# Optimization experiments

Measured on AMD Instinct MI355X. Metric: run time of the kernel, lower is better.

## Reference

```python
import jax, jax.numpy as jnp
import numpy as np

B, T, IN, H, OUT = 1024, 1024, 1, 20, 2
G = 4 * H  # gate dim (i, f, g, o order as in PyTorch)


def setup_inputs() -> dict:
    key = jax.random.key(0)
    ks = jax.random.split(key, 16)
    s = 1.0 / np.sqrt(H)  # PyTorch default uniform(-1/sqrt(H), 1/sqrt(H)) scale
    def u(k, shape):
        return jax.random.uniform(k, shape, jnp.float32, -s, s)
    inp = {"x": jax.random.normal(ks[0], (B, T, IN), jnp.float32)}
    ins = [IN, H, H]
    i = 1
    for l in range(3):
        inp[f"w_ih{l}"] = u(ks[i], (G, ins[l])); i += 1
        inp[f"w_hh{l}"] = u(ks[i], (G, H)); i += 1
        inp[f"b_ih{l}"] = u(ks[i], (G,)); i += 1
        inp[f"b_hh{l}"] = u(ks[i], (G,)); i += 1
    inp["fc_w"] = u(ks[13], (OUT, H))
    inp["fc_b"] = u(ks[14], (OUT,))
    return inp


def _lstm_layer(x, w_ih, w_hh, b_ih, b_hh):
    # x: [B, T, in] -> hidden sequence [B, T, H]
    b, t, _ = x.shape
    h = w_hh.shape[1]
    # Precompute input contribution for all timesteps (vectorized over T).
    xg = jnp.einsum('bti,gi->btg', x, w_ih) + b_ih + b_hh  # [B, T, 4H]

    def step(carry, xg_t):
        hp, cp = carry
        gates = xg_t + hp @ w_hh.T  # [B, 4H]
        i, f, g, o = jnp.split(gates, 4, axis=-1)
        c = jax.nn.sigmoid(f) * cp + jax.nn.sigmoid(i) * jnp.tanh(g)
        hn = jax.nn.sigmoid(o) * jnp.tanh(c)
        return (hn, c), hn

    h0 = jnp.zeros((b, h), x.dtype)
    (_, _), hs = jax.lax.scan(step, (h0, h0), jnp.swapaxes(xg, 0, 1))
    return jnp.swapaxes(hs, 0, 1)  # [B, T, H]


def reference(x, w_ih0, w_hh0, b_ih0, b_hh0, w_ih1, w_hh1, b_ih1, b_hh1,
              w_ih2, w_hh2, b_ih2, b_hh2, fc_w, fc_b):
    y = _lstm_layer(x, w_ih0, w_hh0, b_ih0, b_hh0)
    y = _lstm_layer(y, w_ih1, w_hh1, b_ih1, b_hh1)
    y = _lstm_layer(y, w_ih2, w_hh2, b_ih2, b_hh2)
    return y[:, -1, :] @ fc_w.T + fc_b  # [B, OUT]
```

## Files before the change

kernel.cpp:

```cpp
#include <hip/hip_runtime.h>

typedef _Float16 half2v __attribute__((ext_vector_type(2)));
typedef _Float16 f16x8  __attribute__((ext_vector_type(8)));
typedef float    f32x4  __attribute__((ext_vector_type(4)));

#define T_LEN 1024
#define NBATCH 1024
#define HID 20
#define G_B 2
#define STEPS 8
#define RSLOT 64
#define PPITCH 84

#if defined(__has_builtin)
#if __has_builtin(__builtin_amdgcn_fdot2)
#define HAVE_FDOT2 1
#endif
#endif

#define NLOG2E  -1.4426950408889634f
#define N2LOG2E -2.8853900817779268f

__device__ __forceinline__ float fdot2_(half2v a, half2v b, float c) {
#ifdef HAVE_FDOT2
    return __builtin_amdgcn_fdot2(a, b, c, false);
#else
    return c + (float)a[0] * (float)b[0] + (float)a[1] * (float)b[1];
#endif
}

__device__ __forceinline__ half2v pack2(float a, float b) {
    half2v r; r[0] = (_Float16)a; r[1] = (_Float16)b; return r;
}

__device__ __forceinline__ void load_h20(const _Float16* row, half2v hp[10]) {
    uint4 q0 = *(const uint4*)(row);
    uint4 q1 = *(const uint4*)(row + 8);
    uint2 q2 = *(const uint2*)(row + 16);
    hp[0] = __builtin_bit_cast(half2v, q0.x);
    hp[1] = __builtin_bit_cast(half2v, q0.y);
    hp[2] = __builtin_bit_cast(half2v, q0.z);
    hp[3] = __builtin_bit_cast(half2v, q0.w);
    hp[4] = __builtin_bit_cast(half2v, q1.x);
    hp[5] = __builtin_bit_cast(half2v, q1.y);
    hp[6] = __builtin_bit_cast(half2v, q1.z);
    hp[7] = __builtin_bit_cast(half2v, q1.w);
    hp[8] = __builtin_bit_cast(half2v, q2.x);
    hp[9] = __builtin_bit_cast(half2v, q2.y);
}

__device__ __forceinline__ float dot20s(const half2v W[10], const half2v h[10],
                                        float seed) {
    float a0 = seed, a1 = 0.f;
#pragma unroll
    for (int k = 0; k < 5; ++k) {
        a0 = fdot2_(W[k],     h[k],     a0);
        a1 = fdot2_(W[k + 5], h[k + 5], a1);
    }
    return a0 + a1;
}

__global__ void __launch_bounds__(192, 2) lstm3_r16(
    const float* __restrict__ x,
    const float* __restrict__ wih0, const float* __restrict__ whh0,
    const float* __restrict__ bih0, const float* __restrict__ bhh0,
    const float* __restrict__ wih1, const float* __restrict__ whh1,
    const float* __restrict__ bih1, const float* __restrict__ bhh1,
    const float* __restrict__ wih2, const float* __restrict__ whh2,
    const float* __restrict__ bih2, const float* __restrict__ bhh2,
    const float* __restrict__ fcw, const float* __restrict__ fcb,
    float* __restrict__ out)
{
    __shared__ __align__(16) float xlds[G_B * T_LEN];
    __shared__ __align__(16) _Float16 rings[3][2 * STEPS][RSLOT];
    __shared__ __align__(16) float plds[2][2 * STEPS][PPITCH];

    const int tid = threadIdx.x;
    const int wv = tid / 64;
    const int lane = tid & 63;
    const long b_base = (long)blockIdx.x * G_B;

    {
        const float* xg = x + b_base * T_LEN;
        for (int i = tid; i < G_B * T_LEN; i += 192) {
            const int t = i & (T_LEN - 1);
            const int g = i >> 10;
            xlds[2 * t + g] = xg[i];
        }
        for (int i = tid; i < 3 * 2 * STEPS * RSLOT; i += 192)
            ((_Float16*)rings)[i] = (_Float16)0.0f;
    }

    const bool act = lane < G_B * HID;
    const int g = act ? (lane / HID) : 0;
    const int j = act ? (lane % HID) : 0;

    const float* whh = (wv == 0) ? whh0 : (wv == 1) ? whh1 : whh2;
    const float* wih = (wv == 0) ? wih0 : (wv == 1) ? wih1 : wih2;
    const float* bih = (wv == 0) ? bih0 : (wv == 1) ? bih1 : bih2;
    const float* bhh = (wv == 0) ? bhh0 : (wv == 1) ? bhh1 : bhh2;

    half2v Whh[4][10];
    float bias[4];
    float wx[4] = {0.f, 0.f, 0.f, 0.f};
#pragma unroll
    for (int gt = 0; gt < 4; ++gt) {
        const float sc = (gt == 2) ? N2LOG2E : NLOG2E;
        const int r = gt * HID + j;
#pragma unroll
        for (int k4 = 0; k4 < 5; ++k4) {
            float4 v = *(const float4*)(whh + r * HID + 4 * k4);
            Whh[gt][2 * k4]     = pack2(sc * v.x, sc * v.y);
            Whh[gt][2 * k4 + 1] = pack2(sc * v.z, sc * v.w);
        }
        bias[gt] = sc * (bih[r] + bhh[r]);
        if (wv == 0) wx[gt] = sc * wih[r];
    }

    f16x8 WihB[5];
    if (wv > 0) {
        const int kc = (lane >> 4) * 8;
        const int col = lane & 15;
#pragma unroll
        for (int t = 0; t < 5; ++t) {
            const int n = t * 16 + col;
            const int gt = n / HID;
            const float sc = (gt == 2) ? N2LOG2E : NLOG2E;
            f16x8 v;
#pragma unroll
            for (int e = 0; e < 8; ++e) {
                const int k = kc + e;
                const float w = (k < HID) ? wih[n * HID + k] : 0.f;
                v[e] = (_Float16)(sc * w);
            }
            WihB[t] = v;
        }
    }

    _Float16* const own_base = &rings[wv][0][0];
    const _Float16* const bel_base = (wv > 0) ? &rings[wv - 1][0][0]
                                              : &rings[0][0][0];
    float* const myp = &plds[(wv > 0) ? (wv - 1) : 0][0][0];

    float c = 0.0f;
    float oA[4] = {bias[0], bias[1], bias[2], bias[3]};

    __syncthreads();

    const int SS = T_LEN / STEPS;

    for (int s = 0; s < SS + 2; ++s) {
        const int m = s - wv;
        if (m >= 0 && m < SS) {
            const int t0 = STEPS * m;
            const int hb = (m & 1) * (STEPS * RSLOT);

            if (wv > 0) {
                const int ar = lane & 15;
                const _Float16* ab = bel_base + hb + (ar >> 1) * RSLOT
                                   + (ar & 1) * 32 + (lane >> 4) * 8;
                const f16x8 af = *(const f16x8*)ab;
                const int crow = (lane >> 4) * 4;
                const int ccol = lane & 15;
                const f32x4 z = {0.f, 0.f, 0.f, 0.f};
#pragma unroll
                for (int t = 0; t < 5; ++t) {
                    f32x4 acc = __builtin_amdgcn_mfma_f32_16x16x32_f16(
                        af, WihB[t], z, 0, 0, 0);
#pragma unroll
                    for (int q = 0; q < 4; ++q)
                        myp[(crow + q) * PPITCH + t * 16 + ccol] = acc[q];
                }
            }

            const int qo = hb + g * 32;
#pragma unroll
            for (int i = 0; i < STEPS; ++i) {
                float p[4];
                if (wv == 0) {
                    const float xt = xlds[2 * (t0 + i) + g];
#pragma unroll
                    for (int gt = 0; gt < 4; ++gt)
                        p[gt] = oA[gt] + wx[gt] * xt;
                } else {
                    const float* pr = myp + (2 * i + g) * PPITCH + j;
#pragma unroll
                    for (int gt = 0; gt < 4; ++gt)
                        p[gt] = oA[gt] + pr[gt * HID];
                }
                const float ei = __builtin_exp2f(p[0]);
                const float ef = __builtin_exp2f(p[1]);
                const float eg = __builtin_exp2f(p[2]);
                const float eo = __builtin_exp2f(p[3]);
                const float sf = __builtin_amdgcn_rcpf(1.0f + ef);
                const float u  = (1.0f - eg) *
                    __builtin_amdgcn_rcpf((1.0f + ei) * (1.0f + eg));
                c = sf * c + u;
                const float ec = __builtin_exp2f(N2LOG2E * c);
                const float hn = (1.0f - ec) *
                    __builtin_amdgcn_rcpf((1.0f + eo) * (1.0f + ec));
                _Float16* const wp = own_base + qo + i * RSLOT;
                if (act) wp[j] = (_Float16)hn;
                half2v ho[10];
                load_h20(wp, ho);
#pragma unroll
                for (int gt = 0; gt < 4; ++gt)
                    oA[gt] = dot20s(Whh[gt], ho, bias[gt]);
            }
        }
        __syncthreads();
    }

    if (wv == 2 && lane < 2 * G_B) {
        const int gg = lane >> 1, o = lane & 1;
        float acc = fcb[o];
        const _Float16* h2 = &rings[2][15][gg * 32];
#pragma unroll
        for (int k = 0; k < HID; ++k) {
            acc += fcw[o * HID + k] * (float)h2[k];
        }
        out[(b_base + gg) * 2 + o] = acc;
    }
}

extern "C" void kernel_launch(void* const* d_in, const int* in_sizes, int n_in,
                              void* d_out, int out_size, void* d_ws, size_t ws_size,
                              hipStream_t stream) {
    const float* x    = (const float*)d_in[0];
    const float* wih0 = (const float*)d_in[1];
    const float* whh0 = (const float*)d_in[2];
    const float* bih0 = (const float*)d_in[3];
    const float* bhh0 = (const float*)d_in[4];
    const float* wih1 = (const float*)d_in[5];
    const float* whh1 = (const float*)d_in[6];
    const float* bih1 = (const float*)d_in[7];
    const float* bhh1 = (const float*)d_in[8];
    const float* wih2 = (const float*)d_in[9];
    const float* whh2 = (const float*)d_in[10];
    const float* bih2 = (const float*)d_in[11];
    const float* bhh2 = (const float*)d_in[12];
    const float* fcw  = (const float*)d_in[13];
    const float* fcb  = (const float*)d_in[14];

    lstm3_r16<<<dim3(NBATCH / G_B), dim3(192), 0, stream>>>(
        x, wih0, whh0, bih0, bhh0,
        wih1, whh1, bih1, bhh1,
        wih2, whh2, bih2, bhh2,
        fcw, fcb, (float*)d_out);
}
```

Baseline: 573.8 us.

## Double pipeline chunk to 16 steps and prefetch per-step gate inputs into registers

```diff
diff --git a/kernel.cpp b/kernel.cpp
--- a/kernel.cpp
+++ b/kernel.cpp
@@ -8,7 +8,7 @@
 #define NBATCH 1024
 #define HID 20
 #define G_B 2
-#define STEPS 8
+#define STEPS 16
 #define RSLOT 64
 #define PPITCH 84
 
@@ -60,7 +60,7 @@
     return a0 + a1;
 }
 
-__global__ void __launch_bounds__(192, 2) lstm3_r16(
+__global__ void __launch_bounds__(192, 2) lstm3_r18(
     const float* __restrict__ x,
     const float* __restrict__ wih0, const float* __restrict__ whh0,
     const float* __restrict__ bih0, const float* __restrict__ bhh0,
@@ -118,6 +118,7 @@
     }
 
     f16x8 WihB[5];
+    int col4[5];
     if (wv > 0) {
         const int kc = (lane >> 4) * 8;
         const int col = lane & 15;
@@ -134,6 +135,7 @@
                 v[e] = (_Float16)(sc * w);
             }
             WihB[t] = v;
+            col4[t] = (n % HID) * 4 + gt;
         }
     }
 
@@ -141,6 +143,7 @@
     const _Float16* const bel_base = (wv > 0) ? &rings[wv - 1][0][0]
                                               : &rings[0][0][0];
     float* const myp = &plds[(wv > 0) ? (wv - 1) : 0][0][0];
+    const float* const prb = myp + g * PPITCH + 4 * j;
 
     float c = 0.0f;
     float oA[4] = {bias[0], bias[1], bias[2], bias[3]};
@@ -155,22 +158,37 @@
             const int t0 = STEPS * m;
             const int hb = (m & 1) * (STEPS * RSLOT);
 
+            float xr[STEPS];
+            f32x4 pf[STEPS];
+
             if (wv > 0) {
                 const int ar = lane & 15;
-                const _Float16* ab = bel_base + hb + (ar >> 1) * RSLOT
-                                   + (ar & 1) * 32 + (lane >> 4) * 8;
-                const f16x8 af = *(const f16x8*)ab;
+                const int kc = (lane >> 4) * 8;
                 const int crow = (lane >> 4) * 4;
-                const int ccol = lane & 15;
                 const f32x4 z = {0.f, 0.f, 0.f, 0.f};
 #pragma unroll
-                for (int t = 0; t < 5; ++t) {
-                    f32x4 acc = __builtin_amdgcn_mfma_f32_16x16x32_f16(
-                        af, WihB[t], z, 0, 0, 0);
-#pragma unroll
-                    for (int q = 0; q < 4; ++q)
-                        myp[(crow + q) * PPITCH + t * 16 + ccol] = acc[q];
+                for (int h = 0; h < 2; ++h) {
+                    const _Float16* ab = bel_base + hb
+                        + ((ar >> 1) + 8 * h) * RSLOT + (ar & 1) * 32 + kc;
+                    const f16x8 af = *(const f16x8*)ab;
+#pragma unroll
+                    for (int t = 0; t < 5; ++t) {
+                        f32x4 acc = __builtin_amdgcn_mfma_f32_16x16x32_f16(
+                            af, WihB[t], z, 0, 0, 0);
+                        float* wrow = myp + (crow + 16 * h) * PPITCH + col4[t];
+#pragma unroll
+                        for (int q = 0; q < 4; ++q)
+                            wrow[q * PPITCH] = acc[q];
+                    }
                 }
+#pragma unroll
+                for (int i = 0; i < STEPS; ++i)
+                    pf[i] = *(const f32x4*)(prb + 2 * i * PPITCH);
+            } else {
+                const float* xp = xlds + 2 * t0 + g;
+#pragma unroll
+                for (int i = 0; i < STEPS; ++i)
+                    xr[i] = xp[2 * i];
             }
 
             const int qo = hb + g * 32;
@@ -178,15 +196,13 @@
             for (int i = 0; i < STEPS; ++i) {
                 float p[4];
                 if (wv == 0) {
-                    const float xt = xlds[2 * (t0 + i) + g];
 #pragma unroll
                     for (int gt = 0; gt < 4; ++gt)
-                        p[gt] = oA[gt] + wx[gt] * xt;
+                        p[gt] = oA[gt] + wx[gt] * xr[i];
                 } else {
-                    const float* pr = myp + (2 * i + g) * PPITCH + j;
 #pragma unroll
                     for (int gt = 0; gt < 4; ++gt)
-                        p[gt] = oA[gt] + pr[gt * HID];
+                        p[gt] = oA[gt] + pf[i][gt];
                 }
                 const float ei = __builtin_exp2f(p[0]);
                 const float ef = __builtin_exp2f(p[1]);
@@ -214,7 +230,7 @@
     if (wv == 2 && lane < 2 * G_B) {
         const int gg = lane >> 1, o = lane & 1;
         float acc = fcb[o];
-        const _Float16* h2 = &rings[2][15][gg * 32];
+        const _Float16* h2 = &rings[2][2 * STEPS - 1][gg * 32];
 #pragma unroll
         for (int k = 0; k < HID; ++k) {
             acc += fcw[o * HID + k] * (float)h2[k];
@@ -242,7 +258,7 @@
     const float* fcw  = (const float*)d_in[13];
     const float* fcb  = (const float*)d_in[14];
 
-    lstm3_r16<<<dim3(NBATCH / G_B), dim3(192), 0, stream>>>(
+    lstm3_r18<<<dim3(NBATCH / G_B), dim3(192), 0, stream>>>(
         x, wih0, whh0, bih0, bhh0,
         wih1, whh1, bih1, bhh1,
         wih2, whh2, bih2, bhh2,
```

Measured after the change: 557.8 us. -2.8%, faster.

## Run all three LSTM layers in one wavefront with per-step wavefront skew

Applied to the files above, without the earlier changes.

```diff
diff --git a/kernel.cpp b/kernel.cpp
--- a/kernel.cpp
+++ b/kernel.cpp
@@ -8,8 +8,6 @@
 #define NBATCH 1024
 #define HID 20
 #define G_B 2
-#define STEPS 8
-#define RSLOT 64
 #define PPITCH 84
 
 #if defined(__has_builtin)
@@ -60,7 +58,7 @@
     return a0 + a1;
 }
 
-__global__ void __launch_bounds__(192, 2) lstm3_r16(
+__global__ void __launch_bounds__(64, 1) lstm3_r25(
     const float* __restrict__ x,
     const float* __restrict__ wih0, const float* __restrict__ whh0,
     const float* __restrict__ bih0, const float* __restrict__ bhh0,
@@ -71,154 +69,183 @@
     const float* __restrict__ fcw, const float* __restrict__ fcb,
     float* __restrict__ out)
 {
-    __shared__ __align__(16) float xlds[G_B * T_LEN];
-    __shared__ __align__(16) _Float16 rings[3][2 * STEPS][RSLOT];
-    __shared__ __align__(16) float plds[2][2 * STEPS][PPITCH];
-
-    const int tid = threadIdx.x;
-    const int wv = tid / 64;
-    const int lane = tid & 63;
+    __shared__ __align__(16) float xs[G_B * T_LEN];
+    __shared__ __align__(16) _Float16 hbuf[3][2][G_B * 32];
+    __shared__ __align__(16) float pbuf[2][G_B][PPITCH];
+
+    const int lane = threadIdx.x;
     const long b_base = (long)blockIdx.x * G_B;
 
     {
         const float* xg = x + b_base * T_LEN;
-        for (int i = tid; i < G_B * T_LEN; i += 192) {
+        for (int i = lane; i < G_B * T_LEN; i += 64) {
             const int t = i & (T_LEN - 1);
             const int g = i >> 10;
-            xlds[2 * t + g] = xg[i];
-        }
-        for (int i = tid; i < 3 * 2 * STEPS * RSLOT; i += 192)
-            ((_Float16*)rings)[i] = (_Float16)0.0f;
+            xs[2 * t + g] = xg[i];
+        }
+        for (int i = lane; i < 3 * 2 * G_B * 32; i += 64)
+            ((_Float16*)hbuf)[i] = (_Float16)0.0f;
     }
 
     const bool act = lane < G_B * HID;
     const int g = act ? (lane / HID) : 0;
     const int j = act ? (lane % HID) : 0;
 
-    const float* whh = (wv == 0) ? whh0 : (wv == 1) ? whh1 : whh2;
-    const float* wih = (wv == 0) ? wih0 : (wv == 1) ? wih1 : wih2;
-    const float* bih = (wv == 0) ? bih0 : (wv == 1) ? bih1 : bih2;
-    const float* bhh = (wv == 0) ? bhh0 : (wv == 1) ? bhh1 : bhh2;
-
-    half2v Whh[4][10];
-    float bias[4];
-    float wx[4] = {0.f, 0.f, 0.f, 0.f};
-#pragma unroll
-    for (int gt = 0; gt < 4; ++gt) {
-        const float sc = (gt == 2) ? N2LOG2E : NLOG2E;
-        const int r = gt * HID + j;
-#pragma unroll
-        for (int k4 = 0; k4 < 5; ++k4) {
-            float4 v = *(const float4*)(whh + r * HID + 4 * k4);
-            Whh[gt][2 * k4]     = pack2(sc * v.x, sc * v.y);
-            Whh[gt][2 * k4 + 1] = pack2(sc * v.z, sc * v.w);
-        }
-        bias[gt] = sc * (bih[r] + bhh[r]);
-        if (wv == 0) wx[gt] = sc * wih[r];
-    }
-
-    f16x8 WihB[5];
-    if (wv > 0) {
+    const float* whhs[3] = {whh0, whh1, whh2};
+    const float* wihs[3] = {wih0, wih1, wih2};
+    const float* bihs[3] = {bih0, bih1, bih2};
+    const float* bhhs[3] = {bhh0, bhh1, bhh2};
+
+    half2v Whh[3][4][10];
+    float  bias[3][4];
+    float  wx[4];
+#pragma unroll
+    for (int l = 0; l < 3; ++l) {
+#pragma unroll
+        for (int gt = 0; gt < 4; ++gt) {
+            const float sc = (gt == 2) ? N2LOG2E : NLOG2E;
+            const int r = gt * HID + j;
+#pragma unroll
+            for (int k4 = 0; k4 < 5; ++k4) {
+                float4 v = *(const float4*)(whhs[l] + r * HID + 4 * k4);
+                Whh[l][gt][2 * k4]     = pack2(sc * v.x, sc * v.y);
+                Whh[l][gt][2 * k4 + 1] = pack2(sc * v.z, sc * v.w);
+            }
+            bias[l][gt] = sc * (bihs[l][r] + bhhs[l][r]);
+        }
+    }
+#pragma unroll
+    for (int gt = 0; gt < 4; ++gt)
+        wx[gt] = ((gt == 2) ? N2LOG2E : NLOG2E) * wih0[gt * HID + j];
+
+    f16x8 WihB[2][5];
+    int col4[5];
+    {
         const int kc = (lane >> 4) * 8;
-        const int col = lane & 15;
+        const int coln = lane & 15;
 #pragma unroll
         for (int t = 0; t < 5; ++t) {
-            const int n = t * 16 + col;
-            const int gt = n / HID;
-            const float sc = (gt == 2) ? N2LOG2E : NLOG2E;
-            f16x8 v;
-#pragma unroll
-            for (int e = 0; e < 8; ++e) {
-                const int k = kc + e;
-                const float w = (k < HID) ? wih[n * HID + k] : 0.f;
-                v[e] = (_Float16)(sc * w);
-            }
-            WihB[t] = v;
-        }
-    }
-
-    _Float16* const own_base = &rings[wv][0][0];
-    const _Float16* const bel_base = (wv > 0) ? &rings[wv - 1][0][0]
-                                              : &rings[0][0][0];
-    float* const myp = &plds[(wv > 0) ? (wv - 1) : 0][0][0];
-
-    float c = 0.0f;
-    float oA[4] = {bias[0], bias[1], bias[2], bias[3]};
-
-    __syncthreads();
-
-    const int SS = T_LEN / STEPS;
-
-    for (int s = 0; s < SS + 2; ++s) {
-        const int m = s - wv;
-        if (m >= 0 && m < SS) {
-            const int t0 = STEPS * m;
-            const int hb = (m & 1) * (STEPS * RSLOT);
-
-            if (wv > 0) {
-                const int ar = lane & 15;
-                const _Float16* ab = bel_base + hb + (ar >> 1) * RSLOT
-                                   + (ar & 1) * 32 + (lane >> 4) * 8;
-                const f16x8 af = *(const f16x8*)ab;
-                const int crow = (lane >> 4) * 4;
-                const int ccol = lane & 15;
-                const f32x4 z = {0.f, 0.f, 0.f, 0.f};
+            const int n = t * 16 + coln;
+            const int gtn = n / HID;
+            const float sc = (gtn == 2) ? N2LOG2E : NLOG2E;
+            col4[t] = (n % HID) * 4 + gtn;
+#pragma unroll
+            for (int l = 0; l < 2; ++l) {
+                f16x8 v;
+#pragma unroll
+                for (int e = 0; e < 8; ++e) {
+                    const int k = kc + e;
+                    v[e] = (_Float16)((k < HID) ? sc * wihs[l + 1][n * HID + k]
+                                                : 0.f);
+                }
+                WihB[l][t] = v;
+            }
+        }
+    }
+
+    const int aoff = (lane & 1) * 32 + (lane >> 4) * 8;
+    const int hoo  = g * 32;
+
+    float c0 = 0.f, c1 = 0.f, c2 = 0.f;
+    const f32x4 z = {0.f, 0.f, 0.f, 0.f};
+
+    auto cell = [&](const float p[4], float& c) -> float {
+        const float ei = __builtin_exp2f(p[0]);
+        const float ef = __builtin_exp2f(p[1]);
+        const float eg = __builtin_exp2f(p[2]);
+        const float eo = __builtin_exp2f(p[3]);
+        const float sf = __builtin_amdgcn_rcpf(1.0f + ef);
+        const float u  = (1.0f - eg) *
+            __builtin_amdgcn_rcpf((1.0f + ei) * (1.0f + eg));
+        c = sf * c + u;
+        const float ec = __builtin_exp2f(N2LOG2E * c);
+        return (1.0f - ec) *
+            __builtin_amdgcn_rcpf((1.0f + eo) * (1.0f + ec));
+    };
+
+    auto body = [&](int n) {
+        const int wr = n & 1;
+        const int rd = wr ^ 1;
+        {
+            half2v ho[10];
+            load_h20(&hbuf[0][rd][hoo], ho);
+            const int tx = (n < T_LEN) ? n : (T_LEN - 1);
+            const float xt = xs[2 * tx + g];
+            float p[4];
+#pragma unroll
+            for (int gt = 0; gt < 4; ++gt)
+                p[gt] = dot20s(Whh[0][gt], ho, bias[0][gt]) + wx[gt] * xt;
+            const float hn = cell(p, c0);
+            if (act) hbuf[0][wr][hoo + j] = (_Float16)hn;
+        }
+        {
+            const f16x8 af = *(const f16x8*)(&hbuf[0][rd][0] + aoff);
+            f32x4 acc[5];
+#pragma unroll
+            for (int t = 0; t < 5; ++t)
+                acc[t] = __builtin_amdgcn_mfma_f32_16x16x32_f16(
+                    af, WihB[0][t], z, 0, 0, 0);
+            if (lane < 16) {
 #pragma unroll
                 for (int t = 0; t < 5; ++t) {
-                    f32x4 acc = __builtin_amdgcn_mfma_f32_16x16x32_f16(
-                        af, WihB[t], z, 0, 0, 0);
-#pragma unroll
-                    for (int q = 0; q < 4; ++q)
-                        myp[(crow + q) * PPITCH + t * 16 + ccol] = acc[q];
+                    pbuf[0][0][col4[t]] = acc[t][0];
+                    pbuf[0][1][col4[t]] = acc[t][1];
                 }
             }
-
-            const int qo = hb + g * 32;
-#pragma unroll
-            for (int i = 0; i < STEPS; ++i) {
-                float p[4];
-                if (wv == 0) {
-                    const float xt = xlds[2 * (t0 + i) + g];
-#pragma unroll
-                    for (int gt = 0; gt < 4; ++gt)
-                        p[gt] = oA[gt] + wx[gt] * xt;
-                } else {
-                    const float* pr = myp + (2 * i + g) * PPITCH + j;
-#pragma unroll
-                    for (int gt = 0; gt < 4; ++gt)
-                        p[gt] = oA[gt] + pr[gt * HID];
+            half2v ho[10];
+            load_h20(&hbuf[1][rd][hoo], ho);
+            const f32x4 pf = *(const f32x4*)&pbuf[0][g][4 * j];
+            float p[4];
+#pragma unroll
+            for (int gt = 0; gt < 4; ++gt)
+                p[gt] = dot20s(Whh[1][gt], ho, bias[1][gt]) + pf[gt];
+            const float hn = cell(p, c1);
+            if (act) hbuf[1][wr][hoo + j] = (_Float16)hn;
+        }
+        {
+            const f16x8 af = *(const f16x8*)(&hbuf[1][rd][0] + aoff);
+            f32x4 acc[5];
+#pragma unroll
+            for (int t = 0; t < 5; ++t)
+                acc[t] = __builtin_amdgcn_mfma_f32_16x16x32_f16(
+                    af, WihB[1][t], z, 0, 0, 0);
+            if (lane < 16) {
+#pragma unroll
+                for (int t = 0; t < 5; ++t) {
+                    pbuf[1][0][col4[t]] = acc[t][0];
+                    pbuf[1][1][col4[t]] = acc[t][1];
                 }
-                const float ei = __builtin_exp2f(p[0]);
-                const float ef = __builtin_exp2f(p[1]);
-                const float eg = __builtin_exp2f(p[2]);
-                const float eo = __builtin_exp2f(p[3]);
-                const float sf = __builtin_amdgcn_rcpf(1.0f + ef);
-                const float u  = (1.0f - eg) *
-                    __builtin_amdgcn_rcpf((1.0f + ei) * (1.0f + eg));
-                c = sf * c + u;
-                const float ec = __builtin_exp2f(N2LOG2E * c);
-                const float hn = (1.0f - ec) *
-                    __builtin_amdgcn_rcpf((1.0f + eo) * (1.0f + ec));
-                _Float16* const wp = own_base + qo + i * RSLOT;
-                if (act) wp[j] = (_Float16)hn;
-                half2v ho[10];
-                load_h20(wp, ho);
-#pragma unroll
-                for (int gt = 0; gt < 4; ++gt)
-                    oA[gt] = dot20s(Whh[gt], ho, bias[gt]);
-            }
-        }
-        __syncthreads();
-    }
-
-    if (wv == 2 && lane < 2 * G_B) {
+            }
+            half2v ho[10];
+            load_h20(&hbuf[2][rd][hoo], ho);
+            const f32x4 pf = *(const f32x4*)&pbuf[1][g][4 * j];
+            float p[4];
+#pragma unroll
+            for (int gt = 0; gt < 4; ++gt)
+                p[gt] = dot20s(Whh[2][gt], ho, bias[2][gt]) + pf[gt];
+            const float hn = cell(p, c2);
+            if (act) hbuf[2][wr][hoo + j] = (_Float16)hn;
+        }
+    };
+
+    body(0);
+    c1 = 0.f; c2 = 0.f;
+    if (act) hbuf[1][0][hoo + j] = (_Float16)0.0f;
+    body(1);
+    c2 = 0.f;
+    if (act) hbuf[2][1][hoo + j] = (_Float16)0.0f;
+
+#pragma unroll 1
+    for (int n = 2; n < T_LEN + 2; ++n)
+        body(n);
+
+    if (lane < 2 * G_B) {
         const int gg = lane >> 1, o = lane & 1;
         float acc = fcb[o];
-        const _Float16* h2 = &rings[2][15][gg * 32];
-#pragma unroll
-        for (int k = 0; k < HID; ++k) {
+        const _Float16* h2 = &hbuf[2][(T_LEN + 1) & 1][gg * 32];
+#pragma unroll
+        for (int k = 0; k < HID; ++k)
             acc += fcw[o * HID + k] * (float)h2[k];
-        }
         out[(b_base + gg) * 2 + o] = acc;
     }
 }
@@ -242,7 +269,7 @@
     const float* fcw  = (const float*)d_in[13];
     const float* fcb  = (const float*)d_in[14];
 
-    lstm3_r16<<<dim3(NBATCH / G_B), dim3(192), 0, stream>>>(
+    lstm3_r25<<<dim3(NBATCH / G_B), dim3(64), 0, stream>>>(
         x, wih0, whh0, bih0, bhh0,
         wih1, whh1, bih1, bhh1,
         wih2, whh2, bih2, bhh2,
```

After: 1.192 ms. 108% more time.
